# Kernel tuning notes

Hardware: AMD Instinct MI355X
Metric: run time of the kernel (lower is better)

Reference implementation:

```python
import jax, jax.numpy as jnp
import numpy as np

N_NODES = 100000
N_EDGES = 1600000
IN_DIM = 128
HEADS = 4
HEAD_DIM = 16  # hidden_dim 64 // 4 heads
HID = HEADS * HEAD_DIM
NEG_SLOPE = 0.2


def setup_inputs() -> dict:
    key = jax.random.key(0)
    ks = jax.random.split(key, 20)
    inp = {
        "x": jax.random.normal(ks[0], (N_NODES, IN_DIM), dtype=jnp.float32),
        "edge_index": jax.random.randint(ks[1], (2, N_EDGES), 0, N_NODES, dtype=jnp.int32),
    }
    dims = [IN_DIM, HID, HID]
    for l in range(3):
        d_in = dims[l]
        sc = 1.0 / np.sqrt(d_in)
        inp[f"w{l}"] = jax.random.normal(ks[2 + 4 * l], (d_in, HID), dtype=jnp.float32) * sc
        inp[f"asrc{l}"] = jax.random.normal(ks[3 + 4 * l], (HEADS, HEAD_DIM), dtype=jnp.float32) * 0.1
        inp[f"adst{l}"] = jax.random.normal(ks[4 + 4 * l], (HEADS, HEAD_DIM), dtype=jnp.float32) * 0.1
        inp[f"b{l}"] = jnp.zeros((HID,), dtype=jnp.float32)
    inp["out_w"] = jax.random.normal(ks[14], (HID, 1), dtype=jnp.float32) * (1.0 / np.sqrt(HID))
    inp["out_b"] = jnp.zeros((1,), dtype=jnp.float32)
    return inp


def _gat_layer(h, src, dst, W, a_src, a_dst, b):
    # h: [N, d_in]; src/dst: [E'] (self-loops already appended)
    n = h.shape[0]
    xh = (h @ W).reshape(n, HEADS, HEAD_DIM)              # [N,H,C]
    al_s = jnp.sum(xh * a_src, axis=-1)                   # [N,H]
    al_d = jnp.sum(xh * a_dst, axis=-1)                   # [N,H]
    e = jax.nn.leaky_relu(al_s[src] + al_d[dst], NEG_SLOPE)  # [E',H]
    # segment-softmax over incoming edges of each destination node
    m = jax.ops.segment_max(e, dst, num_segments=n)       # [N,H]
    p = jnp.exp(e - m[dst])
    z = jax.ops.segment_sum(p, dst, num_segments=n)       # [N,H]
    alpha = p / (z[dst] + 1e-16)                          # [E',H]
    msg = xh[src] * alpha[:, :, None]                     # [E',H,C]
    out = jax.ops.segment_sum(msg, dst, num_segments=n)   # [N,H,C]
    return out.reshape(n, HID) + b


def reference(x, edge_index, w0, asrc0, adst0, b0, w1, asrc1, adst1, b1,
              w2, asrc2, adst2, b2, out_w, out_b):
    n = x.shape[0]
    loops = jnp.arange(n, dtype=edge_index.dtype)
    src = jnp.concatenate([edge_index[0], loops])  # PyG GATConv adds self-loops
    dst = jnp.concatenate([edge_index[1], loops])
    h = x
    params = [(w0, asrc0, adst0, b0), (w1, asrc1, adst1, b1), (w2, asrc2, adst2, b2)]
    for W, a_s, a_d, b in params:
        h = _gat_layer(h, src, dst, W, a_s, a_d, b)
        h = jax.nn.relu(h)
    return (h @ out_w + out_b).squeeze(-1)  # [N]
```

## Files before the change

kernel.cpp:

```cpp
#include <hip/hip_runtime.h>


#define NBMAX 512
#define SCHUNK 4096
#define BCAP 8192
#define PADSLACK 768
#define NBH 256

typedef __attribute__((ext_vector_type(8))) short bf16x8;
typedef __attribute__((ext_vector_type(4))) float f32x4;
typedef _Float16 half_t;
typedef __attribute__((ext_vector_type(8))) _Float16 half8;

__device__ inline unsigned short bf16_rtn(float x) {
    union { float f; unsigned u; } a; a.f = x;
    return (unsigned short)((a.u + 0x7FFFu + ((a.u >> 16) & 1u)) >> 16);
}
__device__ inline float bf16_to_f(unsigned short s) {
    union { unsigned u; float f; } b; b.u = ((unsigned)s) << 16;
    return b.f;
}

__global__ __launch_bounds__(256) void k_prep(const float* __restrict__ w0, const float* __restrict__ w1,
                                              const float* __restrict__ w2,
                                              unsigned short* __restrict__ p0h, unsigned short* __restrict__ p0l,
                                              unsigned short* __restrict__ p1h, unsigned short* __restrict__ p1l,
                                              unsigned short* __restrict__ p2h, unsigned short* __restrict__ p2l,
                                              int* __restrict__ bhist, const int* __restrict__ dst, int e,
                                              float* __restrict__ als, half_t* __restrict__ xh16, int n) {
    __shared__ unsigned int h[NBMAX];
    int bid = blockIdx.x, t = threadIdx.x;
    if (bid == 8) {
        if (t < 4) als[(size_t)n * 4 + t] = -1e30f;
        if (t < 64) xh16[(size_t)n * 64 + t] = (half_t)0.f;
        return;
    }
    if (bid >= 9) {
        int bb = bid - 9;
        h[t] = 0;
        h[t + 256] = 0;
        __syncthreads();
        for (int i = bb * 256 + t; i < e; i += NBH * 256)
            atomicAdd(&h[dst[i] >> 8], 1u);
        __syncthreads();
        if (h[t]) atomicAdd(&bhist[t], (int)h[t]);
        if (h[t + 256]) atomicAdd(&bhist[t + 256], (int)h[t + 256]);
        return;
    }
    int g = bid * 256 + t;
    const float* W;
    unsigned short *ph, *pl;
    int idx;
    if (g < 1024) { W = w0; ph = p0h; pl = p0l; idx = g; }
    else if (g < 1536) { W = w1; ph = p1h; pl = p1l; idx = g - 1024; }
    else if (g < 2048) { W = w2; ph = p2h; pl = p2l; idx = g - 1536; }
    else return;
    int ko = idx >> 6, nn = idx & 63;
#pragma unroll
    for (int j = 0; j < 8; ++j) {
        float w = W[(size_t)(ko * 8 + j) * 64 + nn];
        unsigned short hb = bf16_rtn(w);
        ph[(size_t)idx * 8 + j] = hb;
        pl[(size_t)idx * 8 + j] = bf16_rtn(w - bf16_to_f(hb));
    }
}

__global__ __launch_bounds__(512) void k_bscan(const int* __restrict__ bhist, int* __restrict__ boffs,
                                               int* __restrict__ bfill, int nb, int e) {
    __shared__ int s[NBMAX];
    int t = threadIdx.x;
    int v = (t < nb) ? bhist[t] : 0;
    s[t] = v;
    __syncthreads();
    for (int o = 1; o < 512; o <<= 1) {
        int add = (t >= o) ? s[t - o] : 0;
        __syncthreads();
        s[t] += add;
        __syncthreads();
    }
    boffs[t] = s[t] - v;
    if (t == 511) boffs[512] = s[511];
    bfill[t] = 0;
}

template <int D_IN, bool HALF_IN>
__device__ __forceinline__ void mgemm_wave(const void* __restrict__ hv,
                                           const unsigned short* __restrict__ wph,
                                           const unsigned short* __restrict__ wpl,
                                           const float* __restrict__ asrc, const float* __restrict__ adst,
                                           half_t* __restrict__ xh16, float* __restrict__ als,
                                           float* __restrict__ ald, float* __restrict__ mvec,
                                           int m0, int lane, int n) {
    int quad = lane >> 4, l16 = lane & 15;
    int node_a = m0 + l16;
    int mm = min(node_a, n - 1);

    f32x4 acc[4];
#pragma unroll
    for (int i = 0; i < 4; ++i) acc[i] = (f32x4){0.f, 0.f, 0.f, 0.f};

    constexpr int KSTEPS = D_IN / 32;
#pragma unroll
    for (int s = 0; s < KSTEPS; ++s) {
        float av[8];
        if constexpr (HALF_IN) {
            const half_t* hrow = (const half_t*)hv + (size_t)mm * D_IN + quad * 8;
            half8 hvv = *(const half8*)(hrow + s * 32);
#pragma unroll
            for (int j = 0; j < 8; ++j) av[j] = (float)hvv[j];
        } else {
            const float* hrow = (const float*)hv + (size_t)mm * D_IN + quad * 8;
            float4 a0 = *(const float4*)(hrow + s * 32);
            float4 a1 = *(const float4*)(hrow + s * 32 + 4);
            av[0] = a0.x; av[1] = a0.y; av[2] = a0.z; av[3] = a0.w;
            av[4] = a1.x; av[5] = a1.y; av[6] = a1.z; av[7] = a1.w;
        }
        bf16x8 ahi, alo;
#pragma unroll
        for (int j = 0; j < 8; ++j) {
            unsigned short hb = bf16_rtn(av[j]);
            ahi[j] = (short)hb;
            alo[j] = (short)bf16_rtn(av[j] - bf16_to_f(hb));
        }
        const unsigned short* bbase = wph + ((size_t)((s * 4 + quad) * 64 + l16)) * 8;
        const unsigned short* bbasel = wpl + ((size_t)((s * 4 + quad) * 64 + l16)) * 8;
#pragma unroll
        for (int nt = 0; nt < 4; ++nt) {
            bf16x8 bhi = *(const bf16x8*)(bbase + (size_t)nt * 16 * 8);
            bf16x8 blo = *(const bf16x8*)(bbasel + (size_t)nt * 16 * 8);
            acc[nt] = __builtin_amdgcn_mfma_f32_16x16x32_bf16(ahi, bhi, acc[nt], 0, 0, 0);
            acc[nt] = __builtin_amdgcn_mfma_f32_16x16x32_bf16(ahi, blo, acc[nt], 0, 0, 0);
            acc[nt] = __builtin_amdgcn_mfma_f32_16x16x32_bf16(alo, bhi, acc[nt], 0, 0, 0);
        }
    }
#pragma unroll
    for (int nt = 0; nt < 4; ++nt) {
        float as_l = asrc[nt * 16 + l16];
        float ad_l = adst[nt * 16 + l16];
#pragma unroll
        for (int r = 0; r < 4; ++r) {
            int node = m0 + quad * 4 + r;
            float c = acc[nt][r];
            if (node < n) xh16[(size_t)node * 64 + nt * 16 + l16] = (half_t)c;
            float ps = c * as_l, pd = c * ad_l;
            ps += __shfl_xor(ps, 1, 64); pd += __shfl_xor(pd, 1, 64);
            ps += __shfl_xor(ps, 2, 64); pd += __shfl_xor(pd, 2, 64);
            ps += __shfl_xor(ps, 4, 64); pd += __shfl_xor(pd, 4, 64);
            ps += __shfl_xor(ps, 8, 64); pd += __shfl_xor(pd, 8, 64);
            if (l16 == 0 && node < n) {
                als[node * 4 + nt] = ps;
                ald[node * 4 + nt] = pd;
                float sm = ps + pd;
                mvec[node * 4 + nt] = sm >= 0.f ? sm : 0.2f * sm;
            }
        }
    }
}

__global__ __launch_bounds__(256) void k_mgemm64(const half_t* __restrict__ h,
                                                 const unsigned short* __restrict__ wph,
                                                 const unsigned short* __restrict__ wpl,
                                                 const float* __restrict__ asrc, const float* __restrict__ adst,
                                                 half_t* __restrict__ xh16, float* __restrict__ als,
                                                 float* __restrict__ ald, float* __restrict__ mvec, int n) {
    int t = threadIdx.x;
    int m0 = blockIdx.x * 64 + (t >> 6) * 16;
    mgemm_wave<64, true>(h, wph, wpl, asrc, adst, xh16, als, ald, mvec, m0, t & 63, n);
}

__global__ __launch_bounds__(512) void k_mix1(const int* __restrict__ src, const int* __restrict__ dst,
                                              const int* __restrict__ boffs, int* __restrict__ bfill,
                                              unsigned int* __restrict__ edata, int e, int sb,
                                              const float* __restrict__ x,
                                              const unsigned short* __restrict__ p0h,
                                              const unsigned short* __restrict__ p0l,
                                              const float* __restrict__ asrc, const float* __restrict__ adst,
                                              half_t* __restrict__ xh16, float* __restrict__ als,
                                              float* __restrict__ ald, float* __restrict__ mvec, int n) {
    __shared__ unsigned int hist[NBMAX];
    __shared__ unsigned int loc[NBMAX];
    __shared__ int gbase[NBMAX];
    __shared__ unsigned int stmp[NBMAX];
    __shared__ unsigned int sortbuf[SCHUNK];
    __shared__ int posbuf[SCHUNK];
    int t = threadIdx.x;
    if (blockIdx.x >= sb) {
        int mblk = blockIdx.x - sb;
        int m0 = mblk * 128 + (t >> 6) * 16;
        mgemm_wave<128, false>(x, p0h, p0l, asrc, adst, xh16, als, ald, mvec, m0, t & 63, n);
        return;
    }
    int i0 = blockIdx.x * SCHUNK;
    int cnt = min(SCHUNK, e - i0);
    hist[t] = 0;
    __syncthreads();
    for (int j = t; j < cnt; j += 512) atomicAdd(&hist[dst[i0 + j] >> 8], 1u);
    __syncthreads();
    unsigned int v = hist[t];
    stmp[t] = v;
    __syncthreads();
    for (int o = 1; o < 512; o <<= 1) {
        unsigned int add = (t >= o) ? stmp[t - o] : 0;
        __syncthreads();
        stmp[t] += add;
        __syncthreads();
    }
    loc[t] = stmp[t] - v;
    int gb = 0;
    if (v > 0) gb = atomicAdd(&bfill[t], (int)v);
    gbase[t] = boffs[t] + gb - (int)loc[t];
    hist[t] = loc[t];
    __syncthreads();
    for (int j = t; j < cnt; j += 512) {
        int d = dst[i0 + j];
        int s = src[i0 + j];
        int b = d >> 8;
        unsigned int p = atomicAdd(&hist[b], 1u);
        sortbuf[p] = (unsigned int)s | ((unsigned int)(d & 255) << 24);
        posbuf[p] = gbase[b] + (int)p;
    }
    __syncthreads();
    for (int j = t; j < cnt; j += 512) edata[posbuf[j]] = sortbuf[j];
}

__global__ __launch_bounds__(512) void k_mix2(const unsigned int* __restrict__ edata,
                                              const int* __restrict__ boffs, int* __restrict__ poffs,
                                              int* __restrict__ pend, int* __restrict__ ssrc,
                                              int n, int nb, int mg1,
                                              const float* __restrict__ x,
                                              const unsigned short* __restrict__ p0h,
                                              const unsigned short* __restrict__ p0l,
                                              const float* __restrict__ asrc, const float* __restrict__ adst,
                                              half_t* __restrict__ xh16, float* __restrict__ als,
                                              float* __restrict__ ald, float* __restrict__ mvec) {
    __shared__ unsigned int hist[256];
    __shared__ unsigned int stmp[256];
    __shared__ unsigned int loc2[256];
    __shared__ unsigned int srcbuf[BCAP];
    int t = threadIdx.x;
    if (blockIdx.x >= nb) {
        int mblk = mg1 + (blockIdx.x - nb);
        int m0 = mblk * 128 + (t >> 6) * 16;
        mgemm_wave<128, false>(x, p0h, p0l, asrc, adst, xh16, als, ald, mvec, m0, t & 63, n);
        return;
    }
    int b = blockIdx.x;
    int e0 = boffs[b], e1 = boffs[b + 1];
    int cnt = e1 - e0;
    int pb = e0 + b * PADSLACK;
    if (t < 256) hist[t] = 0;
    __syncthreads();
    for (int j = t; j < cnt; j += 512) atomicAdd(&hist[edata[e0 + j] >> 24], 1u);
    __syncthreads();
    unsigned int v = 0, v4 = 0;
    if (t < 256) {
        v = hist[t];
        v4 = (v + 3u) & ~3u;
        stmp[t] = v4;
    }
    __syncthreads();
    for (int o = 1; o < 256; o <<= 1) {
        unsigned int add = 0;
        if (t < 256 && t >= o) add = stmp[t - o];
        __syncthreads();
        if (t < 256) stmp[t] += add;
        __syncthreads();
    }
    int ptot = (int)stmp[255];
    if (t < 256) {
        loc2[t] = stmp[t] - v4;
        int node = b * 256 + t;
        if (node < n) {
            poffs[node] = pb + (int)loc2[t];
            pend[node] = pb + (int)(loc2[t] + v4);
        }
        hist[t] = loc2[t];
    }
    __syncthreads();
    if (cnt + PADSLACK <= BCAP) {
        for (int j = t; j < cnt; j += 512) {
            unsigned int p = edata[e0 + j];
            unsigned int pos = atomicAdd(&hist[p >> 24], 1u);
            srcbuf[pos] = p & 0xFFFFFFu;
        }
        if (t < 256)
            for (unsigned int k = v; k < v4; ++k) srcbuf[loc2[t] + k] = (unsigned int)n;
        __syncthreads();
        for (int j = t; j < ptot; j += 512) ssrc[pb + j] = (int)srcbuf[j];
    } else {
        for (int j = t; j < cnt; j += 512) {
            unsigned int p = edata[e0 + j];
            unsigned int pos = atomicAdd(&hist[p >> 24], 1u);
            ssrc[pb + (int)pos] = (int)(p & 0xFFFFFFu);
        }
        if (t < 256)
            for (unsigned int k = v; k < v4; ++k) ssrc[pb + (int)(loc2[t] + k)] = n;
    }
}

__device__ inline float4 lrelu4(float4 v) {
    float4 r;
    r.x = v.x >= 0.f ? v.x : 0.2f * v.x;
    r.y = v.y >= 0.f ? v.y : 0.2f * v.y;
    r.z = v.z >= 0.f ? v.z : 0.2f * v.z;
    r.w = v.w >= 0.f ? v.w : 0.2f * v.w;
    return r;
}

#define ACCUM(LO, HI, ACCA, ACCB, ZS)                                           \
    {                                                                           \
        int g_ = ((LO) - s0) >> 2, gb_ = ((HI) - s0) >> 2;                      \
        for (; g_ + 4 <= gb_; g_ += 4) {                                        \
            int4 uu0 = *(const int4*)&ub[g_ * 4];                               \
            int4 uu1 = *(const int4*)&ub[g_ * 4 + 4];                           \
            int4 uu2 = *(const int4*)&ub[g_ * 4 + 8];                           \
            int4 uu3 = *(const int4*)&ub[g_ * 4 + 12];                          \
            float4 pp0 = *(const float4*)&per[g_ * 4];                          \
            float4 pp1 = *(const float4*)&per[g_ * 4 + 4];                      \
            float4 pp2 = *(const float4*)&per[g_ * 4 + 8];                      \
            float4 pp3 = *(const float4*)&per[g_ * 4 + 12];                     \
            float x0 = (float)*(const half_t*)(xl + (size_t)(unsigned)uu0.x);   \
            float x1 = (float)*(const half_t*)(xl + (size_t)(unsigned)uu0.y);   \
            float x2 = (float)*(const half_t*)(xl + (size_t)(unsigned)uu0.z);   \
            float x3 = (float)*(const half_t*)(xl + (size_t)(unsigned)uu0.w);   \
            float x4 = (float)*(const half_t*)(xl + (size_t)(unsigned)uu1.x);   \
            float x5 = (float)*(const half_t*)(xl + (size_t)(unsigned)uu1.y);   \
            float x6 = (float)*(const half_t*)(xl + (size_t)(unsigned)uu1.z);   \
            float x7 = (float)*(const half_t*)(xl + (size_t)(unsigned)uu1.w);   \
            float x8 = (float)*(const half_t*)(xl + (size_t)(unsigned)uu2.x);   \
            float x9 = (float)*(const half_t*)(xl + (size_t)(unsigned)uu2.y);   \
            float xa = (float)*(const half_t*)(xl + (size_t)(unsigned)uu2.z);   \
            float xb = (float)*(const half_t*)(xl + (size_t)(unsigned)uu2.w);   \
            float xc = (float)*(const half_t*)(xl + (size_t)(unsigned)uu3.x);   \
            float xd = (float)*(const half_t*)(xl + (size_t)(unsigned)uu3.y);   \
            float xe = (float)*(const half_t*)(xl + (size_t)(unsigned)uu3.z);   \
            float xf = (float)*(const half_t*)(xl + (size_t)(unsigned)uu3.w);   \
            ZS += pp0.x + pp0.y + pp0.z + pp0.w;                                \
            ZS += pp1.x + pp1.y + pp1.z + pp1.w;                                \
            ZS += pp2.x + pp2.y + pp2.z + pp2.w;                                \
            ZS += pp3.x + pp3.y + pp3.z + pp3.w;                                \
            ACCA += pp0.x * x0; ACCB += pp0.y * x1;                             \
            ACCA += pp0.z * x2; ACCB += pp0.w * x3;                             \
            ACCA += pp1.x * x4; ACCB += pp1.y * x5;                             \
            ACCA += pp1.z * x6; ACCB += pp1.w * x7;                             \
            ACCA += pp2.x * x8; ACCB += pp2.y * x9;                             \
            ACCA += pp2.z * xa; ACCB += pp2.w * xb;                             \
            ACCA += pp3.x * xc; ACCB += pp3.y * xd;                             \
            ACCA += pp3.z * xe; ACCB += pp3.w * xf;                             \
        }                                                                       \
        for (; g_ < gb_; ++g_) {                                                \
            int4 uu = *(const int4*)&ub[g_ * 4];                                \
            float4 pp = *(const float4*)&per[g_ * 4];                           \
            float x0 = (float)*(const half_t*)(xl + (size_t)(unsigned)uu.x);    \
            float x1 = (float)*(const half_t*)(xl + (size_t)(unsigned)uu.y);    \
            float x2 = (float)*(const half_t*)(xl + (size_t)(unsigned)uu.z);    \
            float x3 = (float)*(const half_t*)(xl + (size_t)(unsigned)uu.w);    \
            ZS += pp.x + pp.y + pp.z + pp.w;                                    \
            ACCA += pp.x * x0; ACCB += pp.y * x1;                               \
            ACCA += pp.z * x2; ACCB += pp.w * x3;                               \
        }                                                                       \
    }

__global__ __launch_bounds__(256) void k_agg(const half_t* __restrict__ xh16,
                                             const float* __restrict__ als, const float* __restrict__ ald,
                                             const float* __restrict__ mvec,
                                             const int* __restrict__ poffs, const int* __restrict__ pend,
                                             const int* __restrict__ ssrc,
                                             const float* __restrict__ bias, half_t* __restrict__ hout,
                                             const float* __restrict__ outw, const float* __restrict__ outb,
                                             float* __restrict__ fout, int n) {
    __shared__ int s_u[4][64];
    __shared__ float s_pe[4][4][64];
    int wslot = threadIdx.x >> 6;
    int lane = threadIdx.x & 63;
    int w = (blockIdx.x * 256 + threadIdx.x) >> 6;
    int v0 = w << 2;
    if (v0 >= n) return;
    int head = lane >> 4;
    int* ub = s_u[wslot];
    float* per = s_pe[wslot][head];
    float* pew = &s_pe[wslot][0][lane];

    int vlast = n - 1;
    int last = min(v0 + 3, vlast);
    int4 rr = *(const int4*)(poffs + v0);
    int e3 = pend[last];
    int r0 = rr.x;
    int r1 = (v0 + 1 <= last) ? rr.y : e3;
    int r2 = (v0 + 2 <= last) ? rr.z : e3;
    int r3 = (v0 + 3 <= last) ? rr.w : e3;

    const char* xl = (const char*)(xh16 + lane);
    float acc0a = (float)xh16[((size_t)(unsigned)v0 << 6) + lane];
    float acc1a = (float)xh16[((size_t)(unsigned)min(v0 + 1, vlast) << 6) + lane];
    float acc2a = (float)xh16[((size_t)(unsigned)min(v0 + 2, vlast) << 6) + lane];
    float acc3a = (float)xh16[((size_t)(unsigned)min(v0 + 3, vlast) << 6) + lane];
    float acc0b = 0.f, acc1b = 0.f, acc2b = 0.f, acc3b = 0.f;
    float zs0 = 0.f, zs1 = 0.f, zs2 = 0.f, zs3 = 0.f;

    int s0 = r0;
    int u_n = n;
    if (s0 < e3) {
        if (lane < e3 - s0) u_n = ssrc[s0 + lane];
    }
    float4 alu_n = *(const float4*)(als + 4 * (size_t)u_n);
    int e_n = s0 + lane;
    int nid_n = min(v0 + (e_n >= r1) + (e_n >= r2) + (e_n >= r3), vlast);
    float4 ald_n = *(const float4*)(ald + 4 * (size_t)nid_n);
    float4 m_n = *(const float4*)(mvec + 4 * (size_t)nid_n);

    while (s0 < e3) {
        int cnt = min(64, e3 - s0);
        float4 e4 = lrelu4(make_float4(alu_n.x + ald_n.x, alu_n.y + ald_n.y,
                                       alu_n.z + ald_n.z, alu_n.w + ald_n.w));
        float4 pe;
        pe.x = __expf(e4.x - m_n.x);
        pe.y = __expf(e4.y - m_n.y);
        pe.z = __expf(e4.z - m_n.z);
        pe.w = __expf(e4.w - m_n.w);
        ub[lane] = u_n << 7;
        pew[0] = pe.x;
        pew[64] = pe.y;
        pew[128] = pe.z;
        pew[192] = pe.w;
        int s1 = s0 + 64;
        if (s1 < e3) {
            u_n = n;
            if (lane < e3 - s1) u_n = ssrc[s1 + lane];
            alu_n = *(const float4*)(als + 4 * (size_t)u_n);
            int e1 = s1 + lane;
            int nid1 = min(v0 + (e1 >= r1) + (e1 >= r2) + (e1 >= r3), vlast);
            ald_n = *(const float4*)(ald + 4 * (size_t)nid1);
            m_n = *(const float4*)(mvec + 4 * (size_t)nid1);
        }
        int lim = s0 + cnt;
        int hi0 = min(r1, lim);
        int lo1 = max(r1, s0), hi1 = min(r2, lim);
        int lo2 = max(r2, s0), hi2 = min(r3, lim);
        int lo3 = max(r3, s0);
        ACCUM(s0, hi0, acc0a, acc0b, zs0);
        ACCUM(lo1, hi1, acc1a, acc1b, zs1);
        ACCUM(lo2, hi2, acc2a, acc2b, zs2);
        ACCUM(lo3, lim, acc3a, acc3b, zs3);
        s0 = s1;
    }

    float bl = bias[lane];
    float o0 = fmaxf((acc0a + acc0b) / (1.f + zs0 + 1e-16f) + bl, 0.f);
    float o1 = fmaxf((acc1a + acc1b) / (1.f + zs1 + 1e-16f) + bl, 0.f);
    float o2 = fmaxf((acc2a + acc2b) / (1.f + zs2 + 1e-16f) + bl, 0.f);
    float o3 = fmaxf((acc3a + acc3b) / (1.f + zs3 + 1e-16f) + bl, 0.f);
    if (outw) {
        float ow = outw[lane];
        float ob = outb[0];
        float t0 = o0 * ow, t1 = o1 * ow, t2 = o2 * ow, t3 = o3 * ow;
#pragma unroll
        for (int d = 32; d; d >>= 1) {
            t0 += __shfl_down(t0, d, 64);
            t1 += __shfl_down(t1, d, 64);
            t2 += __shfl_down(t2, d, 64);
            t3 += __shfl_down(t3, d, 64);
        }
        if (lane == 0) {
            fout[v0] = t0 + ob;
            if (v0 + 1 < n) fout[v0 + 1] = t1 + ob;
            if (v0 + 2 < n) fout[v0 + 2] = t2 + ob;
            if (v0 + 3 < n) fout[v0 + 3] = t3 + ob;
        }
    } else {
        hout[((size_t)v0 << 6) + lane] = (half_t)o0;
        if (v0 + 1 < n) hout[((size_t)(v0 + 1) << 6) + lane] = (half_t)o1;
        if (v0 + 2 < n) hout[((size_t)(v0 + 2) << 6) + lane] = (half_t)o2;
        if (v0 + 3 < n) hout[((size_t)(v0 + 3) << 6) + lane] = (half_t)o3;
    }
}

extern "C" void kernel_launch(void* const* d_in, const int* in_sizes, int n_in,
                              void* d_out, int out_size, void* d_ws, size_t ws_size,
                              hipStream_t stream) {
    const float* x = (const float*)d_in[0];
    const int* ei = (const int*)d_in[1];
    const float* w[3] = {(const float*)d_in[2], (const float*)d_in[6], (const float*)d_in[10]};
    const float* as[3] = {(const float*)d_in[3], (const float*)d_in[7], (const float*)d_in[11]};
    const float* ad[3] = {(const float*)d_in[4], (const float*)d_in[8], (const float*)d_in[12]};
    const float* b[3] = {(const float*)d_in[5], (const float*)d_in[9], (const float*)d_in[13]};
    const float* outw = (const float*)d_in[14];
    const float* outb = (const float*)d_in[15];

    const int N = in_sizes[0] / 128;
    const int E = in_sizes[1] / 2;
    const int* src = ei;
    const int* dst = ei + E;
    const int NB = (N + 255) / 256;
    const int SB = (E + SCHUNK - 1) / SCHUNK;
    const int GB128 = (N + 127) / 128;
    const int MG1 = (GB128 + 1) / 2;
    const int MG2 = GB128 - MG1;

    char* ws = (char*)d_ws;
    auto alloc = [&](size_t bytes) -> void* {
        void* p = (void*)ws;
        ws += (bytes + 255) & ~(size_t)255;
        return p;
    };
    int* bhist = (int*)alloc(NBMAX * 4);
    int* boffs = (int*)alloc((NBMAX + 1) * 4);
    int* bfill = (int*)alloc(NBMAX * 4);
    int* poffs = (int*)alloc((size_t)(N + 8) * 4);
    int* pend = (int*)alloc((size_t)N * 4);
    int* ssrc = (int*)alloc((size_t)(E + NBMAX * PADSLACK + 256) * 4);
    half_t* xh16 = (half_t*)alloc((size_t)(N + 1) * 64 * 2);
    half_t* hbuf = (half_t*)alloc((size_t)N * 64 * 2);
    float* als = (float*)alloc((size_t)(N + 1) * 4 * 4);
    float* ald = (float*)alloc((size_t)N * 4 * 4);
    float* mvec = (float*)alloc((size_t)N * 4 * 4);
    unsigned short* p0h = (unsigned short*)alloc(8192 * 2);
    unsigned short* p0l = (unsigned short*)alloc(8192 * 2);
    unsigned short* p1h = (unsigned short*)alloc(4096 * 2);
    unsigned short* p1l = (unsigned short*)alloc(4096 * 2);
    unsigned short* p2h = (unsigned short*)alloc(4096 * 2);
    unsigned short* p2l = (unsigned short*)alloc(4096 * 2);
    unsigned int* edata = (unsigned int*)hbuf;

    hipMemsetAsync(bhist, 0, NBMAX * 4, stream);
    k_prep<<<9 + NBH, 256, 0, stream>>>(w[0], w[1], w[2], p0h, p0l, p1h, p1l, p2h, p2l,
                                        bhist, dst, E, als, xh16, N);
    k_bscan<<<1, 512, 0, stream>>>(bhist, boffs, bfill, NB, E);
    k_mix1<<<SB + MG1, 512, 0, stream>>>(src, dst, boffs, bfill, edata, E, SB,
                                         x, p0h, p0l, as[0], ad[0], xh16, als, ald, mvec, N);
    k_mix2<<<NB + MG2, 512, 0, stream>>>(edata, boffs, poffs, pend, ssrc, N, NB, MG1,
                                         x, p0h, p0l, as[0], ad[0], xh16, als, ald, mvec);

    const int gblocks = (N + 63) / 64;
    const int ablocks = (N + 15) / 16;

    k_agg<<<ablocks, 256, 0, stream>>>(xh16, als, ald, mvec, poffs, pend, ssrc, b[0], hbuf, nullptr, nullptr, nullptr, N);
    k_mgemm64<<<gblocks, 256, 0, stream>>>(hbuf, p1h, p1l, as[1], ad[1], xh16, als, ald, mvec, N);
    k_agg<<<ablocks, 256, 0, stream>>>(xh16, als, ald, mvec, poffs, pend, ssrc, b[1], hbuf, nullptr, nullptr, nullptr, N);
    k_mgemm64<<<gblocks, 256, 0, stream>>>(hbuf, p2h, p2l, as[2], ad[2], xh16, als, ald, mvec, N);
    k_agg<<<ablocks, 256, 0, stream>>>(xh16, als, ald, mvec, poffs, pend, ssrc, b[2], nullptr, outw, outb, (float*)d_out, N);
}
```

Baseline: 362.0 us.

## Fuse tail aggregation and GEMM layers into one persistent kernel with grid barriers

```diff
diff --git a/kernel.cpp b/kernel.cpp
--- a/kernel.cpp
+++ b/kernel.cpp
@@ -6,6 +6,7 @@
 #define BCAP 8192
 #define PADSLACK 768
 #define NBH 256
+#define TGRID 1024
 
 typedef __attribute__((ext_vector_type(8))) short bf16x8;
 typedef __attribute__((ext_vector_type(4))) float f32x4;
@@ -27,12 +28,14 @@
                                               unsigned short* __restrict__ p1h, unsigned short* __restrict__ p1l,
                                               unsigned short* __restrict__ p2h, unsigned short* __restrict__ p2l,
                                               int* __restrict__ bhist, const int* __restrict__ dst, int e,
-                                              float* __restrict__ als, half_t* __restrict__ xh16, int n) {
+                                              float* __restrict__ als, half_t* __restrict__ xh16,
+                                              int* __restrict__ gbar, int n) {
     __shared__ unsigned int h[NBMAX];
     int bid = blockIdx.x, t = threadIdx.x;
     if (bid == 8) {
         if (t < 4) als[(size_t)n * 4 + t] = -1e30f;
         if (t < 64) xh16[(size_t)n * 64 + t] = (half_t)0.f;
+        if (t == 64) *gbar = 0;
         return;
     }
     if (bid >= 9) {
@@ -155,17 +158,6 @@
             }
         }
     }
-}
-
-__global__ __launch_bounds__(256) void k_mgemm64(const half_t* __restrict__ h,
-                                                 const unsigned short* __restrict__ wph,
-                                                 const unsigned short* __restrict__ wpl,
-                                                 const float* __restrict__ asrc, const float* __restrict__ adst,
-                                                 half_t* __restrict__ xh16, float* __restrict__ als,
-                                                 float* __restrict__ ald, float* __restrict__ mvec, int n) {
-    int t = threadIdx.x;
-    int m0 = blockIdx.x * 64 + (t >> 6) * 16;
-    mgemm_wave<64, true>(h, wph, wpl, asrc, adst, xh16, als, ald, mvec, m0, t & 63, n);
 }
 
 __global__ __launch_bounds__(512) void k_mix1(const int* __restrict__ src, const int* __restrict__ dst,
@@ -361,20 +353,19 @@
         }                                                                       \
     }
 
-__global__ __launch_bounds__(256) void k_agg(const half_t* __restrict__ xh16,
-                                             const float* __restrict__ als, const float* __restrict__ ald,
-                                             const float* __restrict__ mvec,
-                                             const int* __restrict__ poffs, const int* __restrict__ pend,
-                                             const int* __restrict__ ssrc,
-                                             const float* __restrict__ bias, half_t* __restrict__ hout,
-                                             const float* __restrict__ outw, const float* __restrict__ outb,
-                                             float* __restrict__ fout, int n) {
-    __shared__ int s_u[4][64];
-    __shared__ float s_pe[4][4][64];
+__device__ __forceinline__ void agg_body(int vb, const half_t* __restrict__ xh16,
+                                         const float* __restrict__ als, const float* __restrict__ ald,
+                                         const float* __restrict__ mvec,
+                                         const int* __restrict__ poffs, const int* __restrict__ pend,
+                                         const int* __restrict__ ssrc,
+                                         const float* __restrict__ bias, half_t* __restrict__ hout,
+                                         const float* __restrict__ outw, const float* __restrict__ outb,
+                                         float* __restrict__ fout, int n) {
+    static __shared__ int s_u[4][64];
+    static __shared__ float s_pe[4][4][64];
     int wslot = threadIdx.x >> 6;
     int lane = threadIdx.x & 63;
-    int w = (blockIdx.x * 256 + threadIdx.x) >> 6;
-    int v0 = w << 2;
+    int v0 = ((vb << 2) + wslot) << 2;
     if (v0 >= n) return;
     int head = lane >> 4;
     int* ub = s_u[wslot];
@@ -475,6 +466,50 @@
     }
 }
 
+__device__ __forceinline__ void grid_barrier(int* cnt, int phase) {
+    __syncthreads();
+    if (threadIdx.x == 0) {
+        __threadfence();
+        __hip_atomic_fetch_add(cnt, 1, __ATOMIC_RELEASE, __HIP_MEMORY_SCOPE_AGENT);
+        int target = TGRID * (phase + 1);
+        while (__hip_atomic_load(cnt, __ATOMIC_ACQUIRE, __HIP_MEMORY_SCOPE_AGENT) < target)
+            __builtin_amdgcn_s_sleep(8);
+    }
+    __syncthreads();
+}
+
+__global__ __launch_bounds__(256, 4) void k_tail(const half_t* xh16, half_t* hbuf,
+                                                 float* als, float* ald, float* mvec,
+                                                 const int* poffs, const int* pend, const int* ssrc,
+                                                 const float* b0, const float* b1, const float* b2,
+                                                 const unsigned short* p1h, const unsigned short* p1l,
+                                                 const unsigned short* p2h, const unsigned short* p2l,
+                                                 const float* as1, const float* ad1,
+                                                 const float* as2, const float* ad2,
+                                                 const float* outw, const float* outb,
+                                                 float* fout, int* gbar, int n) {
+    int nvb = (n + 15) / 16;
+    int ngb = (n + 63) / 64;
+    int t = threadIdx.x;
+
+    for (int vb = blockIdx.x; vb < nvb; vb += gridDim.x)
+        agg_body(vb, xh16, als, ald, mvec, poffs, pend, ssrc, b0, hbuf, nullptr, nullptr, nullptr, n);
+    grid_barrier(gbar, 0);
+    for (int mb = blockIdx.x; mb < ngb; mb += gridDim.x)
+        mgemm_wave<64, true>(hbuf, p1h, p1l, as1, ad1, (half_t*)xh16, als, ald, mvec,
+                             mb * 64 + (t >> 6) * 16, t & 63, n);
+    grid_barrier(gbar, 1);
+    for (int vb = blockIdx.x; vb < nvb; vb += gridDim.x)
+        agg_body(vb, xh16, als, ald, mvec, poffs, pend, ssrc, b1, hbuf, nullptr, nullptr, nullptr, n);
+    grid_barrier(gbar, 2);
+    for (int mb = blockIdx.x; mb < ngb; mb += gridDim.x)
+        mgemm_wave<64, true>(hbuf, p2h, p2l, as2, ad2, (half_t*)xh16, als, ald, mvec,
+                             mb * 64 + (t >> 6) * 16, t & 63, n);
+    grid_barrier(gbar, 3);
+    for (int vb = blockIdx.x; vb < nvb; vb += gridDim.x)
+        agg_body(vb, xh16, als, ald, mvec, poffs, pend, ssrc, b2, nullptr, outw, outb, fout, n);
+}
+
 extern "C" void kernel_launch(void* const* d_in, const int* in_sizes, int n_in,
                               void* d_out, int out_size, void* d_ws, size_t ws_size,
                               hipStream_t stream) {
@@ -506,6 +541,7 @@
     int* bhist = (int*)alloc(NBMAX * 4);
     int* boffs = (int*)alloc((NBMAX + 1) * 4);
     int* bfill = (int*)alloc(NBMAX * 4);
+    int* gbar = (int*)alloc(256);
     int* poffs = (int*)alloc((size_t)(N + 8) * 4);
     int* pend = (int*)alloc((size_t)N * 4);
     int* ssrc = (int*)alloc((size_t)(E + NBMAX * PADSLACK + 256) * 4);
@@ -524,19 +560,14 @@
 
     hipMemsetAsync(bhist, 0, NBMAX * 4, stream);
     k_prep<<<9 + NBH, 256, 0, stream>>>(w[0], w[1], w[2], p0h, p0l, p1h, p1l, p2h, p2l,
-                                        bhist, dst, E, als, xh16, N);
+                                        bhist, dst, E, als, xh16, gbar, N);
     k_bscan<<<1, 512, 0, stream>>>(bhist, boffs, bfill, NB, E);
     k_mix1<<<SB + MG1, 512, 0, stream>>>(src, dst, boffs, bfill, edata, E, SB,
                                          x, p0h, p0l, as[0], ad[0], xh16, als, ald, mvec, N);
     k_mix2<<<NB + MG2, 512, 0, stream>>>(edata, boffs, poffs, pend, ssrc, N, NB, MG1,
                                          x, p0h, p0l, as[0], ad[0], xh16, als, ald, mvec);
-
-    const int gblocks = (N + 63) / 64;
-    const int ablocks = (N + 15) / 16;
-
-    k_agg<<<ablocks, 256, 0, stream>>>(xh16, als, ald, mvec, poffs, pend, ssrc, b[0], hbuf, nullptr, nullptr, nullptr, N);
-    k_mgemm64<<<gblocks, 256, 0, stream>>>(hbuf, p1h, p1l, as[1], ad[1], xh16, als, ald, mvec, N);
-    k_agg<<<ablocks, 256, 0, stream>>>(xh16, als, ald, mvec, poffs, pend, ssrc, b[1], hbuf, nullptr, nullptr, nullptr, N);
-    k_mgemm64<<<gblocks, 256, 0, stream>>>(hbuf, p2h, p2l, as[2], ad[2], xh16, als, ald, mvec, N);
-    k_agg<<<ablocks, 256, 0, stream>>>(xh16, als, ald, mvec, poffs, pend, ssrc, b[2], nullptr, outw, outb, (float*)d_out, N);
-}
+    k_tail<<<TGRID, 256, 0, stream>>>(xh16, hbuf, als, ald, mvec, poffs, pend, ssrc,
+                                      b[0], b[1], b[2], p1h, p1l, p2h, p2l,
+                                      as[1], ad[1], as[2], ad[2],
+                                      outw, outb, (float*)d_out, gbar, N);
+}
```

Result: slower. 1.116 ms (+208.3%).
